# Kernel optimization log

Hardware: AMD Instinct MI355X
Metric: run time of the kernel (lower is better)

## Reference

```python
import jax, jax.numpy as jnp
import numpy as np

# LIF constants (LIFParams defaults, normalized units)
V_REST = 0.0
V_TH = 1.0
R = 1.0
DT = 1.0
TAU = 10.0
SLOPE = 5.0  # surrogate heaviside slope

N_INPUT, N_HIDDEN, N_OUTPUT = 784, 256, 10
BATCH, T = 128, 500


def setup_inputs() -> dict:
    key = jax.random.key(0)
    k1, k2, k3 = jax.random.split(key, 3)
    input_spikes = jax.random.uniform(k1, (BATCH, N_INPUT, T), dtype=jnp.float32)
    w_input_hidden = jax.random.uniform(k2, (N_INPUT, N_HIDDEN), dtype=jnp.float32) * 0.1
    w_hidden_output = jax.random.uniform(k3, (N_HIDDEN, N_OUTPUT), dtype=jnp.float32) * 0.1
    return {"input_spikes": input_spikes,
            "w_input_hidden": w_input_hidden,
            "w_hidden_output": w_hidden_output}


def reference(input_spikes, w_input_hidden, w_hidden_output):
    # input_spikes: (B, n_input, T)
    batch = input_spikes.shape[0]
    # relu(weight) computed once (original recomputes per step)
    w_ih = jax.nn.relu(w_input_hidden)
    w_ho = jax.nn.relu(w_hidden_output)
    alpha_h = DT / TAU
    alpha_o = DT / TAU

    xs = jnp.transpose(input_spikes, (2, 0, 1))  # (T, B, n_input)

    def step(carry, x_t):
        v_h, v_o = carry
        I_h = x_t @ w_ih                              # (B, n_hidden)
        v_h = v_h + (-(v_h - V_REST) + R * I_h) * alpha_h
        s_h = jax.nn.sigmoid(SLOPE * (v_h - V_TH))
        I_o = s_h @ w_ho                              # (B, n_output)
        v_o = v_o + (-(v_o - V_REST) + R * I_o) * alpha_o
        s_o = jax.nn.sigmoid(SLOPE * (v_o - V_TH))
        return (v_h, v_o), s_o

    v_h0 = jnp.full((batch, N_HIDDEN), V_REST, dtype=input_spikes.dtype)
    v_o0 = jnp.full((batch, N_OUTPUT), V_REST, dtype=input_spikes.dtype)
    _, out_seq = jax.lax.scan(step, (v_h0, v_o0), xs)   # (T, B, n_output)
    output_spikes = jnp.transpose(out_seq, (1, 2, 0))    # (B, n_output, T)
    firing_rates = output_spikes.mean(axis=2)            # (B, n_output)
    return output_spikes, firing_rates
```

## Files before the change

kernel.cpp:

```cpp
#include <hip/hip_runtime.h>


typedef __attribute__((ext_vector_type(4))) float  floatx4;
typedef __attribute__((ext_vector_type(8))) short  shortx8;
typedef unsigned short u16;
typedef unsigned int   u32;

#define B_   128
#define NIN  784
#define NH   256
#define NO   10
#define T_   500
#define NK   25

__device__ __forceinline__ u16 f2bf(float f) {
    union { float f; u32 u; } x; x.f = f;
    u32 r = x.u + 0x7FFFu + ((x.u >> 16) & 1u);
    return (u16)(r >> 16);
}
__device__ __forceinline__ float bf2f(u16 u) {
    union { u32 u; float f; } x; x.u = ((u32)u) << 16; return x.f;
}
__device__ __forceinline__ float sigmoid5(float v) {
    return 1.0f / (1.0f + __expf(-5.0f * (v - 1.0f)));
}

__device__ __forceinline__ void gload16(const u16* g, u16* l) {
    __builtin_amdgcn_global_load_lds(
        (const __attribute__((address_space(1))) unsigned int*)(const void*)g,
        (__attribute__((address_space(3))) unsigned int*)(void*)l, 16, 0, 0);
}

__global__ void convert_W(const float* __restrict__ w_ih,
                          const float* __restrict__ w_ho,
                          u16* __restrict__ Bt, float* __restrict__ wrelu) {
    if (blockIdx.x == NK * 32) {
        for (int i = threadIdx.x; i < NH * NO; i += 256)
            wrelu[i] = fmaxf(0.f, w_ho[i]);
        return;
    }
    const int k = blockIdx.x;
    const int n = threadIdx.x;
    const float f = (k < NIN) ? fmaxf(0.f, w_ih[k * NH + n]) : 0.f;
    const int kt = k >> 5, kk = k & 31;
    const int slot = (kk >> 3) ^ (n & 3) ^ ((n >> 2) & 3);
    Bt[(size_t)kt * 8192 + n * 32 + slot * 8 + (kk & 7)] = f2bf(f);
}

__global__ __launch_bounds__(512, 4) void gemm_hidden(
    const float* __restrict__ spikes,
    const u16* __restrict__ Bt,
    u16* __restrict__ Ih)
{
    __shared__ u16 SH[24576];
    u16* AS0 = SH;
    u16* AS1 = SH + 4096;
    u16* BS0 = SH + 8192;
    u16* BS1 = SH + 16384;

    const int tid = threadIdx.x;
    const int b   = blockIdx.x >> 2;
    const int tq  = blockIdx.x & 3;
    const int t0  = tq * 128;

    const int kp = tid >> 5, tg = tid & 31;
    const int tloc = t0 + tg * 4;
    const int koff = (2 * kp) & 7;
    const int oct  = kp >> 2;
    const bool t_ok = (tloc <= 496);
    const float* sbase = spikes + (size_t)b * (NIN * T_) + tloc;

    const int lane = tid & 63, wid = tid >> 6;
    const int wm = wid >> 2, wn = wid & 3;
    const int lg = lane >> 4, lr = lane & 15;
    int aOff[4], bOff[4];
#pragma unroll
    for (int mi = 0; mi < 4; ++mi) {
        const int m = wm * 64 + mi * 16 + lr;
        aOff[mi] = m * 32 + ((lg ^ (m & 3) ^ ((m >> 2) & 3)) << 3);
    }
#pragma unroll
    for (int ni = 0; ni < 4; ++ni) {
        const int n = wn * 64 + ni * 16 + lr;
        bOff[ni] = n * 32 + ((lg ^ (n & 3) ^ ((n >> 2) & 3)) << 3);
    }

    floatx4 acc[4][4];
#pragma unroll
    for (int i = 0; i < 4; ++i)
#pragma unroll
        for (int j = 0; j < 4; ++j) acc[i][j] = (floatx4)0.f;

#define LOADA(v0, v1, itv) {                                                   \
        const int gk = (itv) * 32 + 2 * kp;                                    \
        const bool ok0 = t_ok && (gk < NIN);                                   \
        const bool ok1 = t_ok && (gk + 1 < NIN);                               \
        const float* p0 = ok0 ? (sbase + (size_t)gk * T_) : sbase;             \
        const float* p1 = ok1 ? (sbase + (size_t)(gk + 1) * T_) : sbase;       \
        floatx4 u0 = *(const floatx4*)p0;                                      \
        floatx4 u1 = *(const floatx4*)p1;                                      \
        v0 = ok0 ? u0 : (floatx4)0.f;                                          \
        v1 = ok1 ? u1 : (floatx4)0.f; }

#define WRITEA(ASX, v0, v1) { _Pragma("unroll") for (int j = 0; j < 4; ++j) {  \
        const int m = tg * 4 + j;                                              \
        const int slot = oct ^ (m & 3) ^ ((m >> 2) & 3);                       \
        const u32 pk = (u32)f2bf(v0[j]) | ((u32)f2bf(v1[j]) << 16);            \
        *(u32*)&(ASX)[m * 32 + slot * 8 + koff] = pk; } }

#define STAGEB(BSX, itv) { const u16* src = Bt + (size_t)(itv) * 8192;         \
        gload16(src + tid * 8,        (BSX) + tid * 8);                        \
        gload16(src + 4096 + tid * 8, (BSX) + 4096 + tid * 8); }

#define MFMAIT(ASX, BSX) { shortx8 af[4], bf[4];                               \
        _Pragma("unroll") for (int mi = 0; mi < 4; ++mi)                       \
            af[mi] = *(const shortx8*)&(ASX)[aOff[mi]];                        \
        _Pragma("unroll") for (int ni = 0; ni < 4; ++ni)                       \
            bf[ni] = *(const shortx8*)&(BSX)[bOff[ni]];                        \
        _Pragma("unroll") for (int mi = 0; mi < 4; ++mi)                       \
        _Pragma("unroll") for (int ni = 0; ni < 4; ++ni)                       \
            acc[mi][ni] = __builtin_amdgcn_mfma_f32_16x16x32_bf16(             \
                af[mi], bf[ni], acc[mi][ni], 0, 0, 0); }

    floatx4 vaP0, vaP1, vaQ0, vaQ1;

    LOADA(vaP0, vaP1, 0);
    WRITEA(AS0, vaP0, vaP1);
    STAGEB(BS0, 0);
    LOADA(vaQ0, vaQ1, 1);
    __syncthreads();

    for (int it = 0; it < 24; it += 2) {
        WRITEA(AS1, vaQ0, vaQ1);
        STAGEB(BS1, it + 1);
        LOADA(vaP0, vaP1, it + 2);
        MFMAIT(AS0, BS0);
        __syncthreads();
        WRITEA(AS0, vaP0, vaP1);
        STAGEB(BS0, it + 2);
        LOADA(vaQ0, vaQ1, it + 3);
        MFMAIT(AS1, BS1);
        __syncthreads();
    }
    MFMAIT(AS0, BS0);
    __syncthreads();

    u16* Cs = SH;
#pragma unroll
    for (int h = 0; h < 2; ++h) {
        if (wm == h) {
#pragma unroll
            for (int mi = 0; mi < 4; ++mi)
#pragma unroll
                for (int rr = 0; rr < 2; ++rr) {
                    const int mloc = mi * 16 + lg * 4 + rr * 2;
#pragma unroll
                    for (int ni = 0; ni < 4; ++ni) {
                        const int n = wn * 64 + ni * 16 + lr;
                        const u32 pk = (u32)f2bf(acc[mi][ni][rr * 2]) |
                                       ((u32)f2bf(acc[mi][ni][rr * 2 + 1]) << 16);
                        *(u32*)&Cs[n * 64 + (mloc ^ ((n & 7) << 3))] = pk;
                    }
                }
        }
        __syncthreads();
        {
            const int n = tid >> 1, mh = tid & 1;
            u16* gdst = Ih + ((size_t)b * 256 + n) * 512 + t0 + h * 64 + mh * 32;
#pragma unroll
            for (int j = 0; j < 4; ++j) {
                const uint4 v = *(const uint4*)&Cs[n * 64 + ((mh * 32 + 8 * j) ^ ((n & 7) << 3))];
                *(uint4*)(gdst + 8 * j) = v;
            }
        }
        __syncthreads();
    }
#undef LOADA
#undef WRITEA
#undef STAGEB
#undef MFMAIT
}

__global__ __launch_bounds__(512) void scan_h(u16* __restrict__ Ih) {
    const int lane = threadIdx.x & 63;
    const int row  = blockIdx.x * 8 + (threadIdx.x >> 6);
    u16* p = Ih + (size_t)row * 512 + lane * 8;
    shortx8 xv = *(const shortx8*)p;
    float I[8];
#pragma unroll
    for (int j = 0; j < 8; ++j) I[j] = bf2f((u16)xv[j]);
    float z = 0.f;
#pragma unroll
    for (int j = 0; j < 8; ++j) z += (I[j] - z) * 0.1f;
    float A = 0.43046721f, Bv = z;
#pragma unroll
    for (int d = 1; d < 64; d <<= 1) {
        const float Au = __shfl_up(A, d);
        const float Bu = __shfl_up(Bv, d);
        if (lane >= d) { Bv = fmaf(A, Bu, Bv); A *= Au; }
    }
    float v = __shfl_up(Bv, 1);
    if (lane == 0) v = 0.f;
#pragma unroll
    for (int j = 0; j < 8; ++j) {
        v += (I[j] - v) * 0.1f;
        xv[j] = (short)f2bf(sigmoid5(v));
    }
    *(shortx8*)p = xv;
}

__global__ __launch_bounds__(512) void gemm_out(
    const u16* __restrict__ s,
    const float* __restrict__ wr,
    float* __restrict__ Io)
{
    __shared__ float P[4][128][NO];
    const int tid = threadIdx.x;
    const int b   = blockIdx.x >> 2;
    const int tq  = blockIdx.x & 3;
    const int hq  = tid >> 7;
    const int tl  = tid & 127;
    const int t   = tq * 128 + tl;

    float acc[NO];
#pragma unroll
    for (int o = 0; o < NO; ++o) acc[o] = 0.f;
    const u16* sb = s + ((size_t)b * NH + hq * 64) * 512 + t;
    const float* wb = wr + hq * 64 * NO;
#pragma unroll 4
    for (int h = 0; h < 64; ++h) {
        const float sv = bf2f(sb[h * 512]);
#pragma unroll
        for (int o = 0; o < NO; ++o) acc[o] = fmaf(sv, wb[h * NO + o], acc[o]);
    }
#pragma unroll
    for (int o = 0; o < NO; ++o) P[hq][tl][o] = acc[o];
    __syncthreads();

    for (int i = tid; i < 128 * NO; i += 512) {
        const int tt = i / NO, o = i - tt * NO;
        const int tg = tq * 128 + tt;
        if (tg < T_)
            Io[((size_t)b * T_ + tg) * NO + o] =
                P[0][tt][o] + P[1][tt][o] + P[2][tt][o] + P[3][tt][o];
    }
}

__global__ __launch_bounds__(256) void lif_out(
    const float* __restrict__ IoG,
    float* __restrict__ out)
{
    __shared__ float Io[T_ * NO];
    __shared__ float vend[25][NO], vstart[25][NO], psum[25][NO];
    const int b = blockIdx.x, tid = threadIdx.x;

    for (int i = tid; i < T_ * NO; i += 256)
        Io[i] = IoG[(size_t)b * (T_ * NO) + i];
    __syncthreads();

    const int seg = tid / NO, o = tid - seg * NO;
    if (tid < 250) {
        float v = 0.f;
#pragma unroll
        for (int j = 0; j < 20; ++j)
            v += (Io[(seg * 20 + j) * NO + o] - v) * 0.1f;
        vend[seg][o] = v;
    }
    __syncthreads();
    if (tid < NO) {
        float vs = 0.f;
#pragma unroll
        for (int sg = 0; sg < 25; ++sg) {
            vstart[sg][tid] = vs;
            vs = vend[sg][tid] + 0.12157665459f * vs;
        }
    }
    __syncthreads();
    if (tid < 250) {
        float v = vstart[seg][o], ps = 0.f;
#pragma unroll
        for (int j = 0; j < 20; ++j) {
            const int t = seg * 20 + j;
            v += (Io[t * NO + o] - v) * 0.1f;
            const float sv = sigmoid5(v);
            out[(size_t)b * (NO * T_) + (size_t)o * T_ + t] = sv;
            ps += sv;
        }
        psum[seg][o] = ps;
    }
    __syncthreads();
    if (tid < NO) {
        float tot = 0.f;
#pragma unroll
        for (int sg = 0; sg < 25; ++sg) tot += psum[sg][tid];
        out[(size_t)(B_ * NO) * T_ + b * NO + tid] = tot * (1.0f / T_);
    }
}

extern "C" void kernel_launch(void* const* d_in, const int* in_sizes, int n_in,
                              void* d_out, int out_size, void* d_ws, size_t ws_size,
                              hipStream_t stream) {
    (void)in_sizes; (void)n_in; (void)out_size; (void)ws_size;
    const float* spikes = (const float*)d_in[0];
    const float* w_ih   = (const float*)d_in[1];
    const float* w_ho   = (const float*)d_in[2];
    float* out = (float*)d_out;

    float* wrelu = (float*)d_ws;
    u16*   Bt    = (u16*)((char*)d_ws + 16384);
    u16*   Ih    = (u16*)((char*)d_ws + 524288);
    float* Io    = (float*)((char*)d_ws + 524288 + 33554432);

    convert_W  <<<NK * 32 + 1, 256, 0, stream>>>(w_ih, w_ho, Bt, wrelu);
    gemm_hidden<<<512, 512, 0, stream>>>(spikes, Bt, Ih);
    scan_h     <<<4096, 512, 0, stream>>>(Ih);
    gemm_out   <<<512, 512, 0, stream>>>(Ih, wrelu, Io);
    lif_out    <<<B_, 256, 0, stream>>>(Io, out);
}
```

Baseline: 100.0 us.

## Enlarge gemm_hidden tile to 256 timesteps with 1024-thread blocks and finer waits

The hidden GEMM now has each block cover half of the time axis (256 timesteps) with 1024 threads, so each staged B tile is reused by twice as many rows and fewer blocks are launched. Double-buffered A prefetch registers are cut to one set, and __syncthreads is replaced by explicit s_waitcnt vmcnt(2)/lgkmcnt(0) plus s_barrier so in-flight global loads can overlap the barrier. The cost is a grid of only 256 blocks, which may not fill the GPU, plus more LDS and register pressure per block. The last iterations also reload a clamped index, which is redundant work.

```diff
diff --git a/kernel.cpp b/kernel.cpp
--- a/kernel.cpp
+++ b/kernel.cpp
@@ -47,28 +47,28 @@
     Bt[(size_t)kt * 8192 + n * 32 + slot * 8 + (kk & 7)] = f2bf(f);
 }
 
-__global__ __launch_bounds__(512, 4) void gemm_hidden(
+__global__ __launch_bounds__(1024, 4) void gemm_hidden(
     const float* __restrict__ spikes,
     const u16* __restrict__ Bt,
     u16* __restrict__ Ih)
 {
-    __shared__ u16 SH[24576];
+    __shared__ u16 SH[32768];
     u16* AS0 = SH;
-    u16* AS1 = SH + 4096;
-    u16* BS0 = SH + 8192;
-    u16* BS1 = SH + 16384;
+    u16* AS1 = SH + 8192;
+    u16* BS0 = SH + 16384;
+    u16* BS1 = SH + 24576;
 
     const int tid = threadIdx.x;
-    const int b   = blockIdx.x >> 2;
-    const int tq  = blockIdx.x & 3;
-    const int t0  = tq * 128;
-
-    const int kp = tid >> 5, tg = tid & 31;
+    const int b   = blockIdx.x >> 1;
+    const int th  = blockIdx.x & 1;
+    const int t0  = th * 256;
+
+    const int kq = tid >> 6, tg = tid & 63;
     const int tloc = t0 + tg * 4;
-    const int koff = (2 * kp) & 7;
-    const int oct  = kp >> 2;
     const bool t_ok = (tloc <= 496);
     const float* sbase = spikes + (size_t)b * (NIN * T_) + tloc;
+    const int oct  = kq >> 2;
+    const int koff = (2 * kq) & 7;
 
     const int lane = tid & 63, wid = tid >> 6;
     const int wm = wid >> 2, wn = wid & 3;
@@ -92,7 +92,7 @@
         for (int j = 0; j < 4; ++j) acc[i][j] = (floatx4)0.f;
 
 #define LOADA(v0, v1, itv) {                                                   \
-        const int gk = (itv) * 32 + 2 * kp;                                    \
+        const int gk = (itv) * 32 + 2 * kq;                                    \
         const bool ok0 = t_ok && (gk < NIN);                                   \
         const bool ok1 = t_ok && (gk + 1 < NIN);                               \
         const float* p0 = ok0 ? (sbase + (size_t)gk * T_) : sbase;             \
@@ -108,9 +108,8 @@
         const u32 pk = (u32)f2bf(v0[j]) | ((u32)f2bf(v1[j]) << 16);            \
         *(u32*)&(ASX)[m * 32 + slot * 8 + koff] = pk; } }
 
-#define STAGEB(BSX, itv) { const u16* src = Bt + (size_t)(itv) * 8192;         \
-        gload16(src + tid * 8,        (BSX) + tid * 8);                        \
-        gload16(src + 4096 + tid * 8, (BSX) + 4096 + tid * 8); }
+#define STAGEB(BSX, itv)                                                       \
+        gload16(Bt + (size_t)(itv) * 8192 + tid * 8, (BSX) + tid * 8);
 
 #define MFMAIT(ASX, BSX) { shortx8 af[4], bf[4];                               \
         _Pragma("unroll") for (int mi = 0; mi < 4; ++mi)                       \
@@ -122,32 +121,40 @@
             acc[mi][ni] = __builtin_amdgcn_mfma_f32_16x16x32_bf16(             \
                 af[mi], bf[ni], acc[mi][ni], 0, 0, 0); }
 
-    floatx4 vaP0, vaP1, vaQ0, vaQ1;
+#define CBAR2 { asm volatile("s_waitcnt vmcnt(2) lgkmcnt(0)" ::: "memory");    \
+                __builtin_amdgcn_s_barrier(); }
+#define LBAR  { asm volatile("s_waitcnt lgkmcnt(0)" ::: "memory");             \
+                __builtin_amdgcn_s_barrier(); }
+
+    floatx4 vaP0, vaP1;
 
     LOADA(vaP0, vaP1, 0);
     WRITEA(AS0, vaP0, vaP1);
     STAGEB(BS0, 0);
-    LOADA(vaQ0, vaQ1, 1);
-    __syncthreads();
+    LOADA(vaP0, vaP1, 1);
+    CBAR2;
 
     for (int it = 0; it < 24; it += 2) {
-        WRITEA(AS1, vaQ0, vaQ1);
         STAGEB(BS1, it + 1);
-        LOADA(vaP0, vaP1, it + 2);
+        WRITEA(AS1, vaP0, vaP1);
+        { const int nv = (it + 2 < 24) ? (it + 2) : 24;
+          LOADA(vaP0, vaP1, nv); }
         MFMAIT(AS0, BS0);
-        __syncthreads();
+        CBAR2;
+
+        STAGEB(BS0, it + 2);
         WRITEA(AS0, vaP0, vaP1);
-        STAGEB(BS0, it + 2);
-        LOADA(vaQ0, vaQ1, it + 3);
+        { const int nv = (it + 3 < 24) ? (it + 3) : 24;
+          LOADA(vaP0, vaP1, nv); }
         MFMAIT(AS1, BS1);
-        __syncthreads();
+        CBAR2;
     }
     MFMAIT(AS0, BS0);
-    __syncthreads();
+    LBAR;
 
     u16* Cs = SH;
 #pragma unroll
-    for (int h = 0; h < 2; ++h) {
+    for (int h = 0; h < 4; ++h) {
         if (wm == h) {
 #pragma unroll
             for (int mi = 0; mi < 4; ++mi)
@@ -163,22 +170,25 @@
                     }
                 }
         }
-        __syncthreads();
+        LBAR;
         {
-            const int n = tid >> 1, mh = tid & 1;
-            u16* gdst = Ih + ((size_t)b * 256 + n) * 512 + t0 + h * 64 + mh * 32;
-#pragma unroll
-            for (int j = 0; j < 4; ++j) {
-                const uint4 v = *(const uint4*)&Cs[n * 64 + ((mh * 32 + 8 * j) ^ ((n & 7) << 3))];
-                *(uint4*)(gdst + 8 * j) = v;
+            const int n = tid >> 2, ms = tid & 3;
+            u16* gdst = Ih + ((size_t)b * 256 + n) * 512 + t0 + h * 64 + ms * 16;
+#pragma unroll
+            for (int j = 0; j < 2; ++j) {
+                const uint4 v = *(const uint4*)&Cs[n * 64 +
+                                ((ms * 16 + j * 8) ^ ((n & 7) << 3))];
+                *(uint4*)(gdst + j * 8) = v;
             }
         }
-        __syncthreads();
+        LBAR;
     }
 #undef LOADA
 #undef WRITEA
 #undef STAGEB
 #undef MFMAIT
+#undef CBAR2
+#undef LBAR
 }
 
 __global__ __launch_bounds__(512) void scan_h(u16* __restrict__ Ih) {
@@ -312,7 +322,7 @@
     float* Io    = (float*)((char*)d_ws + 524288 + 33554432);
 
     convert_W  <<<NK * 32 + 1, 256, 0, stream>>>(w_ih, w_ho, Bt, wrelu);
-    gemm_hidden<<<512, 512, 0, stream>>>(spikes, Bt, Ih);
+    gemm_hidden<<<256, 1024, 0, stream>>>(spikes, Bt, Ih);
     scan_h     <<<4096, 512, 0, stream>>>(Ih);
     gemm_out   <<<512, 512, 0, stream>>>(Ih, wrelu, Io);
     lif_out    <<<B_, 256, 0, stream>>>(Io, out);
```

Result: faster. 95.49 us (-4.5%).
